# Kernel optimization log

Hardware: AMD Instinct MI355X
Metric: run time of the kernel (lower is better)

Reference implementation:

```python
import jax, jax.numpy as jnp
import numpy as np
from jax import lax

NEG_SLOPE = 0.2
BN_EPS = 1e-5


def _edges(n_nodes, n_total):
    # complete graph (no self loops) on the first n_nodes nodes, as in create_complete_graph,
    # plus PyG GATConv default add_self_loops over ALL n_total nodes.
    i = np.arange(n_nodes)
    src = np.repeat(i, n_nodes)
    dst = np.tile(i, n_nodes)
    keep = src != dst
    loops = np.arange(n_total)
    src = np.concatenate([src[keep], loops]).astype(np.int32)
    dst = np.concatenate([dst[keep], loops]).astype(np.int32)
    return jnp.asarray(src), jnp.asarray(dst)


def _bn_eval(x, g, b, m, v):
    # x: [B, C, H, W]; eval-mode batchnorm with running stats
    inv = g / jnp.sqrt(v + BN_EPS)
    return x * inv[None, :, None, None] + (b - m * inv)[None, :, None, None]


def _gat(x, W, a_src, a_dst, bias, src, dst, n_total):
    h = x @ W                      # [N, D_out]
    s = h @ a_src                  # [N] per-node source score
    d = h @ a_dst                  # [N] per-node dest score
    e = jax.nn.leaky_relu(s[src] + d[dst], NEG_SLOPE)          # [E]
    emax = jax.ops.segment_max(e, dst, num_segments=n_total)   # [N]
    ex = jnp.exp(e - emax[dst])
    denom = jax.ops.segment_sum(ex, dst, num_segments=n_total)
    alpha = ex / denom[dst]                                    # [E]
    out = jax.ops.segment_sum(alpha[:, None] * h[src], dst, num_segments=n_total)
    return out + bias


def setup_inputs() -> dict:
    key = jax.random.key(0)
    ks = jax.random.split(key, 12)
    B, H, W = 8, 64, 64

    def rn(k, shape, s):
        return jax.random.normal(k, shape, jnp.float32) * s

    return {
        "images": jax.random.normal(ks[0], (B, 3, H, W), jnp.float32),
        "conv1_w": rn(ks[1], (64, 3, 3, 3), 0.1), "conv1_b": jnp.zeros((64,), jnp.float32),
        "bn1_g": jnp.ones((64,), jnp.float32), "bn1_b": jnp.zeros((64,), jnp.float32),
        "bn1_m": jnp.zeros((64,), jnp.float32), "bn1_v": jnp.ones((64,), jnp.float32),
        "conv2_w": rn(ks[2], (128, 64, 3, 3), 0.05), "conv2_b": jnp.zeros((128,), jnp.float32),
        "bn2_g": jnp.ones((128,), jnp.float32), "bn2_b": jnp.zeros((128,), jnp.float32),
        "bn2_m": jnp.zeros((128,), jnp.float32), "bn2_v": jnp.ones((128,), jnp.float32),
        "gat1_w": rn(ks[3], (128, 256), 0.05), "gat1_asrc": rn(ks[4], (256,), 0.05),
        "gat1_adst": rn(ks[5], (256,), 0.05), "gat1_bias": jnp.zeros((256,), jnp.float32),
        "gat2_w": rn(ks[6], (256, 128), 0.05), "gat2_asrc": rn(ks[7], (128,), 0.05),
        "gat2_adst": rn(ks[8], (128,), 0.05), "gat2_bias": jnp.zeros((128,), jnp.float32),
        "out_w": rn(ks[9], (128, 10), 0.05), "out_b": jnp.zeros((10,), jnp.float32),
    }


def reference(images, conv1_w, conv1_b, bn1_g, bn1_b, bn1_m, bn1_v,
              conv2_w, conv2_b, bn2_g, bn2_b, bn2_m, bn2_v,
              gat1_w, gat1_asrc, gat1_adst, gat1_bias,
              gat2_w, gat2_asrc, gat2_adst, gat2_bias,
              out_w, out_b):
    dn = ("NCHW", "OIHW", "NCHW")
    x = lax.conv_general_dilated(images, conv1_w, (1, 1), "SAME", dimension_numbers=dn)
    x = x + conv1_b[None, :, None, None]
    x = jax.nn.relu(_bn_eval(x, bn1_g, bn1_b, bn1_m, bn1_v))
    x = lax.reduce_window(x, -jnp.inf, lax.max, (1, 1, 2, 2), (1, 1, 2, 2), "VALID")
    x = lax.conv_general_dilated(x, conv2_w, (1, 1), "SAME", dimension_numbers=dn)
    x = x + conv2_b[None, :, None, None]
    x = jax.nn.relu(_bn_eval(x, bn2_g, bn2_b, bn2_m, bn2_v))

    B = x.shape[0]
    n_nodes = x.shape[2] * x.shape[3]          # (H/2)*(W/2) = 1024
    x = x.reshape(B, 128, n_nodes).transpose(0, 2, 1).reshape(-1, 128)  # [B*n, 128]
    n_total = B * n_nodes
    src, dst = _edges(n_nodes, n_total)

    x = jax.nn.relu(_gat(x, gat1_w, gat1_asrc, gat1_adst, gat1_bias, src, dst, n_total))
    x = jax.nn.relu(_gat(x, gat2_w, gat2_asrc, gat2_adst, gat2_bias, src, dst, n_total))

    x = x.reshape(B, n_nodes, 128).mean(axis=1)   # global_mean_pool over each image's nodes
    logits = x @ out_w + out_b
    return jax.nn.log_softmax(logits, axis=1)
```

## Files before the change

kernel.cpp:

```cpp
#include <hip/hip_runtime.h>
#include <math.h>

#define BN_EPS 1e-5f
#define NEG_SLOPE 0.2f

__device__ __forceinline__ float relu_f(float x) { return x > 0.f ? x : 0.f; }
__device__ __forceinline__ float leaky_f(float z) { return z > 0.f ? z : NEG_SLOPE * z; }

__global__ void conv1_pool(const float* __restrict__ img, const float* __restrict__ w,
                           const float* __restrict__ cb, const float* __restrict__ g,
                           const float* __restrict__ bb, const float* __restrict__ m,
                           const float* __restrict__ vv, float* __restrict__ out)
{
    int blk = blockIdx.x;
    int q = blk & 3, cog = (blk >> 2) & 15, b = blk >> 6;
    int t = threadIdx.x;
    int x = t & 31, y = (q << 3) + (t >> 5);

    float acc[4][4] = {};
#pragma unroll
    for (int ci = 0; ci < 3; ++ci) {
        const float* ib = img + (b * 3 + ci) * 4096;
        float rv[4][4];
#pragma unroll
        for (int r = 0; r < 4; ++r) {
            int yy = 2 * y - 1 + r;
            bool yok = (unsigned)yy < 64u;
            const float* p = ib + yy * 64 + 2 * x;
            float2 c01 = yok ? *(const float2*)p : make_float2(0.f, 0.f);
            rv[r][1] = c01.x;
            rv[r][2] = c01.y;
            rv[r][0] = (yok && x > 0) ? p[-1] : 0.f;
            rv[r][3] = (yok && x < 31) ? p[2] : 0.f;
        }
#pragma unroll
        for (int j = 0; j < 4; ++j) {
            const float* wj = w + ((cog * 4 + j) * 3 + ci) * 9;
#pragma unroll
            for (int ky = 0; ky < 3; ++ky)
#pragma unroll
                for (int kx = 0; kx < 3; ++kx) {
                    float wvv = wj[ky * 3 + kx];
#pragma unroll
                    for (int py = 0; py < 2; ++py)
#pragma unroll
                        for (int px = 0; px < 2; ++px)
                            acc[j][py * 2 + px] += rv[py + ky][px + kx] * wvv;
                }
        }
    }
#pragma unroll
    for (int j = 0; j < 4; ++j) {
        int co = cog * 4 + j;
        float inv = g[co] / sqrtf(vv[co] + BN_EPS);
        float sh = cb[co] * inv + (bb[co] - m[co] * inv);
        float v0 = relu_f(acc[j][0] * inv + sh);
        float v1 = relu_f(acc[j][1] * inv + sh);
        float v2 = relu_f(acc[j][2] * inv + sh);
        float v3 = relu_f(acc[j][3] * inv + sh);
        out[((b * 64 + co) * 32 + y) * 32 + x] = fmaxf(fmaxf(v0, v1), fmaxf(v2, v3));
    }
}

__global__ void conv2_split(const float* __restrict__ in, const float* __restrict__ w,
                            float* __restrict__ c2p)
{
    int blk = blockIdx.x;
    int kz = blk & 1, half = (blk >> 1) & 1, cog = (blk >> 2) & 31, b = blk >> 7;
    int t = threadIdx.x;
    int x2p = (t & 15) * 2;
    int y = half * 16 + (t >> 4);
    bool xnz = x2p != 0;
    bool xhi = x2p == 30;
    const float* ibase = in + b * 65536 + kz * 32768;
    int xb = xnz ? x2p - 1 : 0;

    float acc[4][2] = {};

#pragma unroll 2
    for (int ci = 0; ci < 32; ++ci) {
        const float* cb2 = ibase + ci * 1024;
        float rc[3][4];
#pragma unroll
        for (int r = 0; r < 3; ++r) {
            int yy = y - 1 + r;
            bool yok = (unsigned)yy < 32u;
            const float* p = cb2 + yy * 32 + xb;
            float4 f = yok ? *(const float4*)p : make_float4(0.f, 0.f, 0.f, 0.f);
            rc[r][0] = xnz ? f.x : 0.f;
            rc[r][1] = xnz ? f.y : f.x;
            rc[r][2] = xnz ? f.z : f.y;
            float r3 = xnz ? f.w : f.z;
            rc[r][3] = xhi ? 0.f : r3;
        }
#pragma unroll
        for (int j = 0; j < 4; ++j) {
            const float* wj = w + ((cog * 4 + j) * 64 + kz * 32 + ci) * 9;
#pragma unroll
            for (int ky = 0; ky < 3; ++ky)
#pragma unroll
                for (int kx = 0; kx < 3; ++kx) {
                    float wvv = wj[ky * 3 + kx];
                    acc[j][0] += rc[ky][kx] * wvv;
                    acc[j][1] += rc[ky][kx + 1] * wvv;
                }
        }
    }

    float* pp = c2p + (size_t)kz * 1048576;
    int bid = b * 64 + cog * 2 + half;
    size_t base = ((size_t)bid * 256 + t) * 8;
    float4 s0 = {acc[0][0], acc[1][0], acc[2][0], acc[3][0]};
    float4 s1 = {acc[0][1], acc[1][1], acc[2][1], acc[3][1]};
    *(float4*)&pp[base] = s0;
    *(float4*)&pp[base + 4] = s1;
}

__global__ void conv2_combine(const float* __restrict__ c2p,
                              const float* __restrict__ cb, const float* __restrict__ g,
                              const float* __restrict__ bb, const float* __restrict__ m,
                              const float* __restrict__ vv, float* __restrict__ x0)
{
    int gid = blockIdx.x * 256 + threadIdx.x;
    int t = gid & 255, bid = gid >> 8;
    int half = bid & 1, cog = (bid >> 1) & 31, b = bid >> 6;
    size_t off = (size_t)gid * 8;

    float4 u0 = *(const float4*)&c2p[off];
    float4 u1 = *(const float4*)&c2p[off + 4];
    float4 w0 = *(const float4*)&c2p[1048576 + off];
    float4 w1 = *(const float4*)&c2p[1048576 + off + 4];
    float sx = u0.x + w0.x, sy = u0.y + w0.y, sz = u0.z + w0.z, sw = u0.w + w0.w;
    float qx = u1.x + w1.x, qy = u1.y + w1.y, qz = u1.z + w1.z, qw = u1.w + w1.w;

    float4 gg = ((const float4*)g)[cog];
    float4 vvv = ((const float4*)vv)[cog];
    float4 bbb = ((const float4*)bb)[cog];
    float4 mm = ((const float4*)m)[cog];
    float4 cbb = ((const float4*)cb)[cog];
    float ix = gg.x / sqrtf(vvv.x + BN_EPS);
    float iy = gg.y / sqrtf(vvv.y + BN_EPS);
    float iz = gg.z / sqrtf(vvv.z + BN_EPS);
    float iw = gg.w / sqrtf(vvv.w + BN_EPS);
    float shx = cbb.x * ix + (bbb.x - mm.x * ix);
    float shy = cbb.y * iy + (bbb.y - mm.y * iy);
    float shz = cbb.z * iz + (bbb.z - mm.z * iz);
    float shw = cbb.w * iw + (bbb.w - mm.w * iw);

    float4 o0 = {relu_f(sx * ix + shx), relu_f(sy * iy + shy),
                 relu_f(sz * iz + shz), relu_f(sw * iw + shw)};
    float4 o1 = {relu_f(qx * ix + shx), relu_f(qy * iy + shy),
                 relu_f(qz * iz + shz), relu_f(qw * iw + shw)};

    int y = half * 16 + (t >> 4), x2p = (t & 15) * 2;
    int n0 = b * 1024 + y * 32 + x2p;
    *(float4*)&x0[(size_t)n0 * 128 + cog * 4] = o0;
    *(float4*)&x0[(size_t)(n0 + 1) * 128 + cog * 4] = o1;
}

template <int K, int N, bool SELF, bool SCORE>
__global__ void gemm32(const float* __restrict__ A, const float* __restrict__ Ahi,
                       const float* __restrict__ abias,
                       const float* __restrict__ B, float* __restrict__ C,
                       const float* __restrict__ asrc, const float* __restrict__ adst,
                       float* __restrict__ sp, float* __restrict__ dp)
{
    __shared__ float As[16][33];
    __shared__ float Bs[16][64];
    int t = threadIdx.x;
    int m0 = blockIdx.x * 32;
    int n0 = blockIdx.y * 64;
    int tx = t & 15, ty = t >> 4;
    int am = t >> 3, ak2 = (t & 7) * 2;
    bool hi = SELF && m0 >= 1024;
    const float* Ab = hi ? Ahi : A;
    float acc[2][4] = {};

    for (int k0 = 0; k0 < K; k0 += 16) {
        float2 av = *(const float2*)&Ab[(size_t)(m0 + am) * K + k0 + ak2];
        if (hi) {
            av.x = relu_f(av.x + abias[k0 + ak2]);
            av.y = relu_f(av.y + abias[k0 + ak2 + 1]);
        }
        float4 bv = *(const float4*)&B[(size_t)(k0 + ty) * N + n0 + tx * 4];
        __syncthreads();
        As[ak2][am] = av.x;
        As[ak2 + 1][am] = av.y;
        *(float4*)&Bs[ty][tx * 4] = bv;
        __syncthreads();
#pragma unroll
        for (int kk = 0; kk < 16; ++kk) {
            float a0 = As[kk][ty * 2], a1 = As[kk][ty * 2 + 1];
            float4 b4 = *(const float4*)&Bs[kk][tx * 4];
            acc[0][0] += a0 * b4.x; acc[0][1] += a0 * b4.y;
            acc[0][2] += a0 * b4.z; acc[0][3] += a0 * b4.w;
            acc[1][0] += a1 * b4.x; acc[1][1] += a1 * b4.y;
            acc[1][2] += a1 * b4.z; acc[1][3] += a1 * b4.w;
        }
    }
#pragma unroll
    for (int i = 0; i < 2; ++i) {
        float4 o = {acc[i][0], acc[i][1], acc[i][2], acc[i][3]};
        *(float4*)&C[(size_t)(m0 + ty * 2 + i) * N + n0 + tx * 4] = o;
    }

    if (SCORE && m0 < 1024) {
        float4 as4 = *(const float4*)&asrc[n0 + tx * 4];
        float4 ad4 = *(const float4*)&adst[n0 + tx * 4];
#pragma unroll
        for (int i = 0; i < 2; ++i) {
            float ss = acc[i][0] * as4.x + acc[i][1] * as4.y +
                       acc[i][2] * as4.z + acc[i][3] * as4.w;
            float dd = acc[i][0] * ad4.x + acc[i][1] * ad4.y +
                       acc[i][2] * ad4.z + acc[i][3] * ad4.w;
#pragma unroll
            for (int off = 1; off < 16; off <<= 1) {
                ss += __shfl_xor(ss, off);
                dd += __shfl_xor(dd, off);
            }
            if (tx == 0) {
                sp[blockIdx.y * 1024 + m0 + ty * 2 + i] = ss;
                dp[blockIdx.y * 1024 + m0 + ty * 2 + i] = dd;
            }
        }
    }
}

template <int D, int KS, int NT>
__global__ void gat_agg_gemm(const float* __restrict__ h, const float* __restrict__ sp,
                             const float* __restrict__ dp, float* __restrict__ pacc,
                             float* __restrict__ pden)
{
    __shared__ float Ss[1024];
    __shared__ float As[16][33];
    __shared__ float Bs[16][64];
    __shared__ float red[4];
    __shared__ float part[16][32];

    const int CH = 1024 / KS;
    int t = threadIdx.x;
    int m0 = blockIdx.x * 32;
    int n0 = blockIdx.y * 64;
    int kz = blockIdx.z;
    int tx = t & 15, ty = t >> 4;
    int vg2 = tx * 2;

    float4 sa = {0.f, 0.f, 0.f, 0.f};
#pragma unroll
    for (int nt = 0; nt < NT; ++nt) {
        float4 u = *(const float4*)&sp[nt * 1024 + t * 4];
        sa.x += u.x; sa.y += u.y; sa.z += u.z; sa.w += u.w;
    }
    *(float4*)&Ss[t * 4] = sa;
    float lm = fmaxf(fmaxf(sa.x, sa.y), fmaxf(sa.z, sa.w));
#pragma unroll
    for (int off = 1; off < 64; off <<= 1) lm = fmaxf(lm, __shfl_xor(lm, off));
    if ((t & 63) == 0) red[t >> 6] = lm;
    __syncthreads();
    float smax = fmaxf(fmaxf(red[0], red[1]), fmaxf(red[2], red[3]));

    float dv0 = 0.f, dv1 = 0.f;
#pragma unroll
    for (int nt = 0; nt < NT; ++nt) {
        dv0 += dp[nt * 1024 + m0 + vg2];
        dv1 += dp[nt * 1024 + m0 + vg2 + 1];
    }
    float mv0 = leaky_f(smax + dv0), mv1 = leaky_f(smax + dv1);
    float ds0 = 0.f, ds1 = 0.f;
    float acc[2][4] = {};

    for (int k0 = kz * CH; k0 < kz * CH + CH; k0 += 16) {
        float4 bv = *(const float4*)&h[(size_t)(k0 + ty) * D + n0 + tx * 4];
        float su = Ss[k0 + ty];
        float a0 = __expf(leaky_f(su + dv0) - mv0);
        float a1 = __expf(leaky_f(su + dv1) - mv1);
        ds0 += a0; ds1 += a1;
        __syncthreads();
        As[ty][vg2] = a0;
        As[ty][vg2 + 1] = a1;
        *(float4*)&Bs[ty][tx * 4] = bv;
        __syncthreads();
#pragma unroll
        for (int kk = 0; kk < 16; ++kk) {
            float a0m = As[kk][ty * 2], a1m = As[kk][ty * 2 + 1];
            float4 b4 = *(const float4*)&Bs[kk][tx * 4];
            acc[0][0] += a0m * b4.x; acc[0][1] += a0m * b4.y;
            acc[0][2] += a0m * b4.z; acc[0][3] += a0m * b4.w;
            acc[1][0] += a1m * b4.x; acc[1][1] += a1m * b4.y;
            acc[1][2] += a1m * b4.z; acc[1][3] += a1m * b4.w;
        }
    }

    __syncthreads();
    part[ty][vg2] = ds0;
    part[ty][vg2 + 1] = ds1;
    __syncthreads();

#pragma unroll
    for (int i = 0; i < 2; ++i) {
        float4 o = {acc[i][0], acc[i][1], acc[i][2], acc[i][3]};
        *(float4*)&pacc[((size_t)kz * 1024 + m0 + ty * 2 + i) * D + n0 + tx * 4] = o;
    }
    if (t < 32) {
        float den = 0.f;
#pragma unroll
        for (int u = 0; u < 16; ++u) den += part[u][t];
        pden[kz * 1024 + m0 + t] = den;
    }
}

template <int D, int KS>
__global__ void gat_combine(const float* __restrict__ pacc, const float* __restrict__ pden,
                            const float* __restrict__ bias, float* __restrict__ out)
{
    int idx = blockIdx.x * blockDim.x + threadIdx.x;
    if (idx >= 1024 * D / 4) return;
    int c4 = idx & (D / 4 - 1);
    int v = idx / (D / 4);
    float4 a = {0.f, 0.f, 0.f, 0.f};
    float den = 0.f;
#pragma unroll
    for (int ks = 0; ks < KS; ++ks) {
        float4 p = ((const float4*)pacc)[(size_t)(ks * 1024 + v) * (D / 4) + c4];
        a.x += p.x; a.y += p.y; a.z += p.z; a.w += p.w;
        den += pden[ks * 1024 + v];
    }
    float rd = 1.f / den;
    float4 bz = ((const float4*)bias)[c4];
    float4 o = {relu_f(a.x * rd + bz.x), relu_f(a.y * rd + bz.y),
                relu_f(a.z * rd + bz.z), relu_f(a.w * rd + bz.w)};
    ((float4*)out)[(size_t)v * (D / 4) + c4] = o;
}

__global__ void pool_part(const float* __restrict__ x2, const float* __restrict__ h2,
                          const float* __restrict__ bias2, float* __restrict__ part)
{
    int b = blockIdx.x >> 4, seg = blockIdx.x & 15, t = threadIdx.x;
    float acc = 0.f;
    if (b == 0) {
        const float* p = x2 + ((size_t)seg * 64) * 128 + t;
#pragma unroll 8
        for (int n = 0; n < 64; ++n) acc += p[(size_t)n * 128];
    } else {
        float bz = bias2[t];
        const float* p = h2 + ((size_t)b * 1024 + seg * 64) * 128 + t;
#pragma unroll 8
        for (int n = 0; n < 64; ++n) acc += relu_f(p[(size_t)n * 128] + bz);
    }
    part[(b * 16 + seg) * 128 + t] = acc;
}

__global__ void head_kernel(const float* __restrict__ part, const float* __restrict__ ow,
                            const float* __restrict__ ob, float* __restrict__ out)
{
    __shared__ float pooled[128];
    __shared__ float logits[10];
    int b = blockIdx.x, t = threadIdx.x;
    float acc = 0.f;
#pragma unroll
    for (int sgi = 0; sgi < 16; ++sgi) acc += part[(b * 16 + sgi) * 128 + t];
    pooled[t] = acc * (1.f / 1024.f);
    __syncthreads();
    if (t < 10) {
        float l = ob[t];
        for (int c = 0; c < 128; ++c) l += pooled[c] * ow[c * 10 + t];
        logits[t] = l;
    }
    __syncthreads();
    if (t == 0) {
        float mx = logits[0];
        for (int j = 1; j < 10; ++j) mx = fmaxf(mx, logits[j]);
        float sum = 0.f;
        for (int j = 0; j < 10; ++j) sum += expf(logits[j] - mx);
        float lse = mx + logf(sum);
        for (int j = 0; j < 10; ++j) out[b * 10 + j] = logits[j] - lse;
    }
}

extern "C" void kernel_launch(void* const* d_in, const int* in_sizes, int n_in,
                              void* d_out, int out_size, void* d_ws, size_t ws_size,
                              hipStream_t stream)
{
    const float* images = (const float*)d_in[0];
    const float* c1w = (const float*)d_in[1];
    const float* c1b = (const float*)d_in[2];
    const float* bn1g = (const float*)d_in[3];
    const float* bn1b = (const float*)d_in[4];
    const float* bn1m = (const float*)d_in[5];
    const float* bn1v = (const float*)d_in[6];
    const float* c2w = (const float*)d_in[7];
    const float* c2b = (const float*)d_in[8];
    const float* bn2g = (const float*)d_in[9];
    const float* bn2b = (const float*)d_in[10];
    const float* bn2m = (const float*)d_in[11];
    const float* bn2v = (const float*)d_in[12];
    const float* g1w = (const float*)d_in[13];
    const float* g1as = (const float*)d_in[14];
    const float* g1ad = (const float*)d_in[15];
    const float* g1b = (const float*)d_in[16];
    const float* g2w = (const float*)d_in[17];
    const float* g2as = (const float*)d_in[18];
    const float* g2ad = (const float*)d_in[19];
    const float* g2b = (const float*)d_in[20];
    const float* ow = (const float*)d_in[21];
    const float* ob = (const float*)d_in[22];
    float* out = (float*)d_out;

    float* ws = (float*)d_ws;
    float* x1    = ws;
    float* bufc1 = ws + 2097152;
    float* h1    = ws + 2621440;
    float* x0    = ws + 4718592;
    float* h2    = ws + 5767168;
    float* sp1   = ws + 6815744;
    float* dp1   = ws + 6819840;
    float* sp2   = ws + 6823936;
    float* dp2   = ws + 6825984;
    float* part  = bufc1;
    float* pden1 = bufc1 + 16384;
    float* pden2 = bufc1 + 24576;
    float* pacc1 = x0;
    float* pacc2 = h1;
    float* x2    = x0;
    float* c2p   = x1;

    conv1_pool<<<512, 256, 0, stream>>>(images, c1w, c1b, bn1g, bn1b, bn1m, bn1v, bufc1);
    conv2_split<<<1024, 256, 0, stream>>>(bufc1, c2w, c2p);
    conv2_combine<<<512, 256, 0, stream>>>(c2p, c2b, bn2g, bn2b, bn2m, bn2v, x0);

    gemm32<128, 256, false, true><<<dim3(256, 4), 256, 0, stream>>>(
        x0, x0, nullptr, g1w, h1, g1as, g1ad, sp1, dp1);
    gat_agg_gemm<256, 8, 4><<<dim3(32, 4, 8), 256, 0, stream>>>(h1, sp1, dp1, pacc1, pden1);
    gat_combine<256, 8><<<256, 256, 0, stream>>>(pacc1, pden1, g1b, x1);

    gemm32<256, 128, true, true><<<dim3(256, 2), 256, 0, stream>>>(
        x1, h1, g1b, g2w, h2, g2as, g2ad, sp2, dp2);
    gat_agg_gemm<128, 16, 2><<<dim3(32, 2, 16), 256, 0, stream>>>(h2, sp2, dp2, pacc2, pden2);
    gat_combine<128, 16><<<128, 256, 0, stream>>>(pacc2, pden2, g2b, x2);

    pool_part<<<128, 128, 0, stream>>>(x2, h2, g2b, part);
    head_kernel<<<8, 128, 0, stream>>>(part, ow, ob, out);
}
```

Before: 205.3 us.

## Fuse conv2 and GAT combine steps into downstream GEMM and pooling kernels

Removes the conv2_combine and both gat_combine kernels. The split-K conv reduction with BN and ReLU now happens while loading A in the first GAT GEMM. The GAT1 partial-sum normalization, bias and ReLU happen while loading A in the second GEMM. The GAT2 normalization is folded into the pooling kernel. This cuts three launches and the intermediate buffer round-trips, at the cost of redundant partial-sum reads across column blocks and strided gather loads in the GEMMs. Workspace buffers are rearranged to match.

```diff
diff --git a/kernel.cpp b/kernel.cpp
--- a/kernel.cpp
+++ b/kernel.cpp
@@ -116,73 +116,48 @@
     *(float4*)&pp[base + 4] = s1;
 }
 
-__global__ void conv2_combine(const float* __restrict__ c2p,
-                              const float* __restrict__ cb, const float* __restrict__ g,
-                              const float* __restrict__ bb, const float* __restrict__ m,
-                              const float* __restrict__ vv, float* __restrict__ x0)
-{
-    int gid = blockIdx.x * 256 + threadIdx.x;
-    int t = gid & 255, bid = gid >> 8;
-    int half = bid & 1, cog = (bid >> 1) & 31, b = bid >> 6;
-    size_t off = (size_t)gid * 8;
-
-    float4 u0 = *(const float4*)&c2p[off];
-    float4 u1 = *(const float4*)&c2p[off + 4];
-    float4 w0 = *(const float4*)&c2p[1048576 + off];
-    float4 w1 = *(const float4*)&c2p[1048576 + off + 4];
-    float sx = u0.x + w0.x, sy = u0.y + w0.y, sz = u0.z + w0.z, sw = u0.w + w0.w;
-    float qx = u1.x + w1.x, qy = u1.y + w1.y, qz = u1.z + w1.z, qw = u1.w + w1.w;
-
-    float4 gg = ((const float4*)g)[cog];
-    float4 vvv = ((const float4*)vv)[cog];
-    float4 bbb = ((const float4*)bb)[cog];
-    float4 mm = ((const float4*)m)[cog];
-    float4 cbb = ((const float4*)cb)[cog];
-    float ix = gg.x / sqrtf(vvv.x + BN_EPS);
-    float iy = gg.y / sqrtf(vvv.y + BN_EPS);
-    float iz = gg.z / sqrtf(vvv.z + BN_EPS);
-    float iw = gg.w / sqrtf(vvv.w + BN_EPS);
-    float shx = cbb.x * ix + (bbb.x - mm.x * ix);
-    float shy = cbb.y * iy + (bbb.y - mm.y * iy);
-    float shz = cbb.z * iz + (bbb.z - mm.z * iz);
-    float shw = cbb.w * iw + (bbb.w - mm.w * iw);
-
-    float4 o0 = {relu_f(sx * ix + shx), relu_f(sy * iy + shy),
-                 relu_f(sz * iz + shz), relu_f(sw * iw + shw)};
-    float4 o1 = {relu_f(qx * ix + shx), relu_f(qy * iy + shy),
-                 relu_f(qz * iz + shz), relu_f(qw * iw + shw)};
-
-    int y = half * 16 + (t >> 4), x2p = (t & 15) * 2;
-    int n0 = b * 1024 + y * 32 + x2p;
-    *(float4*)&x0[(size_t)n0 * 128 + cog * 4] = o0;
-    *(float4*)&x0[(size_t)(n0 + 1) * 128 + cog * 4] = o1;
-}
-
-template <int K, int N, bool SELF, bool SCORE>
-__global__ void gemm32(const float* __restrict__ A, const float* __restrict__ Ahi,
-                       const float* __restrict__ abias,
-                       const float* __restrict__ B, float* __restrict__ C,
-                       const float* __restrict__ asrc, const float* __restrict__ adst,
-                       float* __restrict__ sp, float* __restrict__ dp)
+__global__ void gemm1_conv(const float* __restrict__ c2p,
+                           const float* __restrict__ cb, const float* __restrict__ g,
+                           const float* __restrict__ bb, const float* __restrict__ mbn,
+                           const float* __restrict__ vv,
+                           const float* __restrict__ B, float* __restrict__ C,
+                           const float* __restrict__ asrc, const float* __restrict__ adst,
+                           float* __restrict__ sp, float* __restrict__ dp)
 {
     __shared__ float As[16][33];
     __shared__ float Bs[16][64];
+    __shared__ float invs[128];
+    __shared__ float shs[128];
     int t = threadIdx.x;
+    if (t < 128) {
+        float iv = g[t] / sqrtf(vv[t] + BN_EPS);
+        invs[t] = iv;
+        shs[t] = cb[t] * iv + (bb[t] - mbn[t] * iv);
+    }
+
     int m0 = blockIdx.x * 32;
     int n0 = blockIdx.y * 64;
     int tx = t & 15, ty = t >> 4;
     int am = t >> 3, ak2 = (t & 7) * 2;
-    bool hi = SELF && m0 >= 1024;
-    const float* Ab = hi ? Ahi : A;
+    int mm = m0 + am;
+    int b = mm >> 10, rem = mm & 1023, y = rem >> 5, x = rem & 31;
+    int xp = x >> 1, odd = x & 1, half = y >> 4, yy = y & 15;
+    int toff = yy * 16 + xp;
+    size_t cbase = ((size_t)((b * 64 + half) * 256 + toff)) * 8 + odd * 4 + (ak2 & 3)
+                 + (size_t)(ak2 >> 2) * 4096;
+    const float* p0 = c2p + cbase;
+    const float* p1 = c2p + 1048576 + cbase;
+    __syncthreads();
+
     float acc[2][4] = {};
-
-    for (int k0 = 0; k0 < K; k0 += 16) {
-        float2 av = *(const float2*)&Ab[(size_t)(m0 + am) * K + k0 + ak2];
-        if (hi) {
-            av.x = relu_f(av.x + abias[k0 + ak2]);
-            av.y = relu_f(av.y + abias[k0 + ak2 + 1]);
-        }
-        float4 bv = *(const float4*)&B[(size_t)(k0 + ty) * N + n0 + tx * 4];
+    for (int k0 = 0; k0 < 128; k0 += 16) {
+        int k = k0 + ak2;
+        float2 u = *(const float2*)&p0[(size_t)k0 * 1024];
+        float2 w2 = *(const float2*)&p1[(size_t)k0 * 1024];
+        float2 av;
+        av.x = relu_f((u.x + w2.x) * invs[k] + shs[k]);
+        av.y = relu_f((u.y + w2.y) * invs[k + 1] + shs[k + 1]);
+        float4 bv = *(const float4*)&B[(size_t)(k0 + ty) * 256 + n0 + tx * 4];
         __syncthreads();
         As[ak2][am] = av.x;
         As[ak2 + 1][am] = av.y;
@@ -201,10 +176,10 @@
 #pragma unroll
     for (int i = 0; i < 2; ++i) {
         float4 o = {acc[i][0], acc[i][1], acc[i][2], acc[i][3]};
-        *(float4*)&C[(size_t)(m0 + ty * 2 + i) * N + n0 + tx * 4] = o;
-    }
-
-    if (SCORE && m0 < 1024) {
+        *(float4*)&C[(size_t)(m0 + ty * 2 + i) * 256 + n0 + tx * 4] = o;
+    }
+
+    if (m0 < 1024) {
         float4 as4 = *(const float4*)&asrc[n0 + tx * 4];
         float4 ad4 = *(const float4*)&adst[n0 + tx * 4];
 #pragma unroll
@@ -226,6 +201,96 @@
     }
 }
 
+__global__ void gemm2_fused(const float* __restrict__ pacc1, const float* __restrict__ pden1,
+                            const float* __restrict__ b1, const float* __restrict__ h1,
+                            const float* __restrict__ B, float* __restrict__ C,
+                            const float* __restrict__ asrc, const float* __restrict__ adst,
+                            float* __restrict__ sp, float* __restrict__ dp)
+{
+    __shared__ float As[16][33];
+    __shared__ float Bs[16][64];
+    int t = threadIdx.x;
+    int m0 = blockIdx.x * 32;
+    int n0 = blockIdx.y * 64;
+    int tx = t & 15, ty = t >> 4;
+    int am = t >> 3, ak2 = (t & 7) * 2;
+    int mm = m0 + am;
+    bool lo = m0 < 1024;
+
+    float rden = 0.f;
+    const float* ap;
+    if (lo) {
+        float den = 0.f;
+#pragma unroll
+        for (int ks = 0; ks < 8; ++ks) den += pden1[ks * 1024 + mm];
+        rden = 1.f / den;
+        ap = pacc1 + (size_t)mm * 256 + ak2;
+    } else {
+        ap = h1 + (size_t)mm * 256 + ak2;
+    }
+
+    float acc[2][4] = {};
+    for (int k0 = 0; k0 < 256; k0 += 16) {
+        float2 av;
+        float z0 = b1[k0 + ak2], z1 = b1[k0 + ak2 + 1];
+        if (lo) {
+            float sx = 0.f, sy = 0.f;
+#pragma unroll
+            for (int ks = 0; ks < 8; ++ks) {
+                float2 u = *(const float2*)&ap[(size_t)ks * 262144 + k0];
+                sx += u.x; sy += u.y;
+            }
+            av.x = relu_f(sx * rden + z0);
+            av.y = relu_f(sy * rden + z1);
+        } else {
+            float2 u = *(const float2*)&ap[k0];
+            av.x = relu_f(u.x + z0);
+            av.y = relu_f(u.y + z1);
+        }
+        float4 bv = *(const float4*)&B[(size_t)(k0 + ty) * 128 + n0 + tx * 4];
+        __syncthreads();
+        As[ak2][am] = av.x;
+        As[ak2 + 1][am] = av.y;
+        *(float4*)&Bs[ty][tx * 4] = bv;
+        __syncthreads();
+#pragma unroll
+        for (int kk = 0; kk < 16; ++kk) {
+            float a0 = As[kk][ty * 2], a1 = As[kk][ty * 2 + 1];
+            float4 b4 = *(const float4*)&Bs[kk][tx * 4];
+            acc[0][0] += a0 * b4.x; acc[0][1] += a0 * b4.y;
+            acc[0][2] += a0 * b4.z; acc[0][3] += a0 * b4.w;
+            acc[1][0] += a1 * b4.x; acc[1][1] += a1 * b4.y;
+            acc[1][2] += a1 * b4.z; acc[1][3] += a1 * b4.w;
+        }
+    }
+#pragma unroll
+    for (int i = 0; i < 2; ++i) {
+        float4 o = {acc[i][0], acc[i][1], acc[i][2], acc[i][3]};
+        *(float4*)&C[(size_t)(m0 + ty * 2 + i) * 128 + n0 + tx * 4] = o;
+    }
+
+    if (lo) {
+        float4 as4 = *(const float4*)&asrc[n0 + tx * 4];
+        float4 ad4 = *(const float4*)&adst[n0 + tx * 4];
+#pragma unroll
+        for (int i = 0; i < 2; ++i) {
+            float ss = acc[i][0] * as4.x + acc[i][1] * as4.y +
+                       acc[i][2] * as4.z + acc[i][3] * as4.w;
+            float dd = acc[i][0] * ad4.x + acc[i][1] * ad4.y +
+                       acc[i][2] * ad4.z + acc[i][3] * ad4.w;
+#pragma unroll
+            for (int off = 1; off < 16; off <<= 1) {
+                ss += __shfl_xor(ss, off);
+                dd += __shfl_xor(dd, off);
+            }
+            if (tx == 0) {
+                sp[blockIdx.y * 1024 + m0 + ty * 2 + i] = ss;
+                dp[blockIdx.y * 1024 + m0 + ty * 2 + i] = dd;
+            }
+        }
+    }
+}
+
 template <int D, int KS, int NT>
 __global__ void gat_agg_gemm(const float* __restrict__ h, const float* __restrict__ sp,
                              const float* __restrict__ dp, float* __restrict__ pacc,
@@ -309,40 +374,33 @@
     }
 }
 
-template <int D, int KS>
-__global__ void gat_combine(const float* __restrict__ pacc, const float* __restrict__ pden,
-                            const float* __restrict__ bias, float* __restrict__ out)
-{
-    int idx = blockIdx.x * blockDim.x + threadIdx.x;
-    if (idx >= 1024 * D / 4) return;
-    int c4 = idx & (D / 4 - 1);
-    int v = idx / (D / 4);
-    float4 a = {0.f, 0.f, 0.f, 0.f};
-    float den = 0.f;
-#pragma unroll
-    for (int ks = 0; ks < KS; ++ks) {
-        float4 p = ((const float4*)pacc)[(size_t)(ks * 1024 + v) * (D / 4) + c4];
-        a.x += p.x; a.y += p.y; a.z += p.z; a.w += p.w;
-        den += pden[ks * 1024 + v];
-    }
-    float rd = 1.f / den;
-    float4 bz = ((const float4*)bias)[c4];
-    float4 o = {relu_f(a.x * rd + bz.x), relu_f(a.y * rd + bz.y),
-                relu_f(a.z * rd + bz.z), relu_f(a.w * rd + bz.w)};
-    ((float4*)out)[(size_t)v * (D / 4) + c4] = o;
-}
-
-__global__ void pool_part(const float* __restrict__ x2, const float* __restrict__ h2,
-                          const float* __restrict__ bias2, float* __restrict__ part)
-{
-    int b = blockIdx.x >> 4, seg = blockIdx.x & 15, t = threadIdx.x;
+__global__ void pool_combine(const float* __restrict__ pacc2, const float* __restrict__ pden2,
+                             const float* __restrict__ h2, const float* __restrict__ b2,
+                             float* __restrict__ part)
+{
+    __shared__ float dinv[64];
+    int blk = blockIdx.x;
+    int b = blk >> 4, seg = blk & 15, t = threadIdx.x;
+    float bz = b2[t];
     float acc = 0.f;
     if (b == 0) {
-        const float* p = x2 + ((size_t)seg * 64) * 128 + t;
-#pragma unroll 8
-        for (int n = 0; n < 64; ++n) acc += p[(size_t)n * 128];
+        if (t < 64) {
+            int v = seg * 64 + t;
+            float den = 0.f;
+#pragma unroll
+            for (int ks = 0; ks < 16; ++ks) den += pden2[ks * 1024 + v];
+            dinv[t] = 1.f / den;
+        }
+        __syncthreads();
+        for (int n = 0; n < 64; ++n) {
+            int v = seg * 64 + n;
+            float s = 0.f;
+#pragma unroll
+            for (int ks = 0; ks < 16; ++ks)
+                s += pacc2[(size_t)(ks * 1024 + v) * 128 + t];
+            acc += relu_f(s * dinv[n] + bz);
+        }
     } else {
-        float bz = bias2[t];
         const float* p = h2 + ((size_t)b * 1024 + seg * 64) * 128 + t;
 #pragma unroll 8
         for (int n = 0; n < 64; ++n) acc += relu_f(p[(size_t)n * 128] + bz);
@@ -407,37 +465,31 @@
     float* out = (float*)d_out;
 
     float* ws = (float*)d_ws;
-    float* x1    = ws;
-    float* bufc1 = ws + 2097152;
-    float* h1    = ws + 2621440;
-    float* x0    = ws + 4718592;
-    float* h2    = ws + 5767168;
-    float* sp1   = ws + 6815744;
-    float* dp1   = ws + 6819840;
-    float* sp2   = ws + 6823936;
-    float* dp2   = ws + 6825984;
-    float* part  = bufc1;
-    float* pden1 = bufc1 + 16384;
-    float* pden2 = bufc1 + 24576;
-    float* pacc1 = x0;
-    float* pacc2 = h1;
-    float* x2    = x0;
-    float* c2p   = x1;
+    float* c2p   = ws;
+    float* pacc1 = ws;
+    float* h1    = ws + 2097152;
+    float* pacc2 = ws + 2097152;
+    float* bufc1 = ws + 4194304;
+    float* h2    = ws + 4194304;
+    float* sp1   = ws + 5242880;
+    float* dp1   = ws + 5246976;
+    float* sp2   = ws + 5251072;
+    float* dp2   = ws + 5253120;
+    float* pden1 = ws + 5255168;
+    float* pden2 = ws + 5263360;
+    float* part  = ws + 5279744;
 
     conv1_pool<<<512, 256, 0, stream>>>(images, c1w, c1b, bn1g, bn1b, bn1m, bn1v, bufc1);
     conv2_split<<<1024, 256, 0, stream>>>(bufc1, c2w, c2p);
-    conv2_combine<<<512, 256, 0, stream>>>(c2p, c2b, bn2g, bn2b, bn2m, bn2v, x0);
-
-    gemm32<128, 256, false, true><<<dim3(256, 4), 256, 0, stream>>>(
-        x0, x0, nullptr, g1w, h1, g1as, g1ad, sp1, dp1);
+
+    gemm1_conv<<<dim3(256, 4), 256, 0, stream>>>(
+        c2p, c2b, bn2g, bn2b, bn2m, bn2v, g1w, h1, g1as, g1ad, sp1, dp1);
     gat_agg_gemm<256, 8, 4><<<dim3(32, 4, 8), 256, 0, stream>>>(h1, sp1, dp1, pacc1, pden1);
-    gat_combine<256, 8><<<256, 256, 0, stream>>>(pacc1, pden1, g1b, x1);
-
-    gemm32<256, 128, true, true><<<dim3(256, 2), 256, 0, stream>>>(
-        x1, h1, g1b, g2w, h2, g2as, g2ad, sp2, dp2);
+
+    gemm2_fused<<<dim3(256, 2), 256, 0, stream>>>(
+        pacc1, pden1, g1b, h1, g2w, h2, g2as, g2ad, sp2, dp2);
     gat_agg_gemm<128, 16, 2><<<dim3(32, 2, 16), 256, 0, stream>>>(h2, sp2, dp2, pacc2, pden2);
-    gat_combine<128, 16><<<128, 256, 0, stream>>>(pacc2, pden2, g2b, x2);
-
-    pool_part<<<128, 128, 0, stream>>>(x2, h2, g2b, part);
+
+    pool_combine<<<128, 128, 0, stream>>>(pacc2, pden2, h2, g2b, part);
     head_kernel<<<8, 128, 0, stream>>>(part, ow, ob, out);
 }
```

After: 235.1 us. 1.15x slower.
